# Kernel optimization log

Hardware: AMD Instinct MI355X
Metric: run time of the kernel (lower is better)

Reference implementation:

```python
import jax, jax.numpy as jnp
import numpy as np

NINP, NHID, NTOK, NLAYERS, BSZ = 4096, 512, 50257, 2, 32
T_ENC, T_DEC = 80, 40


def lstm_layer(x, h0, c0, Wih, Whh, b):
    """Single LSTM layer over a [T,B,in] sequence; PyTorch gate order i,f,g,o."""
    def step(carry, xt):
        h, c = carry
        z = xt @ Wih.T + h @ Whh.T + b  # [B, 4H]
        i, f, g, o = jnp.split(z, 4, axis=-1)
        c = jax.nn.sigmoid(f) * c + jax.nn.sigmoid(i) * jnp.tanh(g)
        h = jax.nn.sigmoid(o) * jnp.tanh(c)
        return (h, c), h
    (hN, cN), ys = jax.lax.scan(step, (h0, c0), x)
    return ys, hN, cN


def multi_lstm(x, h0, c0, params):
    """Stacked LSTM; params = list of (Wih, Whh, b) per layer."""
    hs, cs = [], []
    y = x
    for l, (Wih, Whh, b) in enumerate(params):
        y, hN, cN = lstm_layer(y, h0[l], c0[l], Wih, Whh, b)
        hs.append(hN); cs.append(cN)
    return y, jnp.stack(hs), jnp.stack(cs)


def setup_inputs():
    key = jax.random.key(0)
    ks = iter(jax.random.split(key, 32))
    def rn(shape, scale=0.05):
        return (jax.random.normal(next(ks), shape, dtype=jnp.float32) * scale)
    H4 = 4 * NHID
    d = {}
    d["inp"] = rn((T_ENC, BSZ, NINP), 1.0)
    for name in ("hid1_h", "hid1_c", "hid2_h", "hid2_c"):
        d[name] = jnp.zeros((NLAYERS, BSZ, NHID), jnp.float32)
    # lstm1: layer0 in=NINP, layer1 in=NHID (b = b_ih + b_hh fused)
    d["l1_Wih0"] = rn((H4, NINP)); d["l1_Whh0"] = rn((H4, NHID)); d["l1_b0"] = rn((H4,))
    d["l1_Wih1"] = rn((H4, NHID)); d["l1_Whh1"] = rn((H4, NHID)); d["l1_b1"] = rn((H4,))
    # lstm2: layer0 in=2*NHID, layer1 in=NHID
    d["l2_Wih0"] = rn((H4, 2 * NHID)); d["l2_Whh0"] = rn((H4, NHID)); d["l2_b0"] = rn((H4,))
    d["l2_Wih1"] = rn((H4, NHID)); d["l2_Whh1"] = rn((H4, NHID)); d["l2_b1"] = rn((H4,))
    d["W_out"] = rn((NTOK, NHID)); d["b_out"] = rn((NTOK,))
    d["W_emb"] = rn((NHID, NTOK)); d["b_emb"] = rn((NHID,))
    d["target_len"] = T_DEC
    return d


def reference(inp, hid1_h, hid1_c, hid2_h, hid2_c,
              l1_Wih0, l1_Whh0, l1_b0, l1_Wih1, l1_Whh1, l1_b1,
              l2_Wih0, l2_Whh0, l2_b0, l2_Wih1, l2_Whh1, l2_b1,
              W_out, b_out, W_emb, b_emb, target_len):
    p1 = [(l1_Wih0, l1_Whh0, l1_b0), (l1_Wih1, l1_Whh1, l1_b1)]
    p2 = [(l2_Wih0, l2_Whh0, l2_b0), (l2_Wih1, l2_Whh1, l2_b1)]
    T, B, ninp = inp.shape
    H = hid1_h.shape[-1]
    # --- encoding stage ---
    out1, h1, c1 = multi_lstm(inp, hid1_h, hid1_c, p1)
    pad_h = jnp.zeros((T, B, H), inp.dtype)
    _, h2, c2 = multi_lstm(jnp.concatenate([pad_h, out1], axis=-1), hid2_h, hid2_c, p2)
    # --- decoding stage ---
    pad_in = jnp.zeros((target_len, B, ninp), inp.dtype)
    out1d, _, _ = multi_lstm(pad_in, h1, c1, p1)
    # vocab2emb(one-hot BOS at index 0) = W_emb[:, 0] + b_emb; never updated in
    # the original loop (variable-name bug), so it is constant over decode steps,
    # making the per-step loop equivalent to one lstm2 scan.
    bos_emb = W_emb[:, 0] + b_emb  # [H]
    bos = jnp.broadcast_to(bos_emb, (target_len, B, H))
    out2d, _, _ = multi_lstm(jnp.concatenate([bos, out1d], axis=-1), h2, c2, p2)
    logits = jnp.einsum('tbh,vh->tbv', out2d, W_out) + b_out  # [T_dec, B, V]
    return jax.nn.log_softmax(logits, axis=-1)
```

## Files before the change

### kernel.cpp

```cpp
#include <hip/hip_runtime.h>
#include <hip/hip_bf16.h>
#include <cstddef>

#define NINP 4096
#define NHID 512
#define G4   2048
#define NTOK 50257
#define BSZ  32
#define T_ENC 80
#define T_DEC 40

typedef __attribute__((ext_vector_type(4))) float  f32x4;
typedef __attribute__((ext_vector_type(4))) __bf16 bf16x4;
typedef __attribute__((ext_vector_type(8))) __bf16 bf16x8;

__device__ __forceinline__ int sw_off(int r, int k) {
    return r * 128 + ((((k >> 3) ^ (r & 7)) << 4) | ((k & 7) << 1));
}
__device__ __forceinline__ int swA(int r, int k) {
    return r * 256 + ((((k >> 3) ^ (r & 7)) << 4) | ((k & 7) << 1));
}
__device__ __forceinline__ int sw512(int r, int k) {
    return r * 1024 + ((((k >> 3) ^ (r & 7)) << 4) | ((k & 7) << 1));
}

__device__ __forceinline__ bf16x4 hi4(const float4& v) {
    bf16x4 h; h[0] = (__bf16)v.x; h[1] = (__bf16)v.y;
    h[2] = (__bf16)v.z; h[3] = (__bf16)v.w; return h;
}

__device__ __forceinline__ void split8(const float4& a, const float4& b,
                                       bf16x8& h, bf16x8& l) {
    float x[8] = {a.x, a.y, a.z, a.w, b.x, b.y, b.z, b.w};
    #pragma unroll
    for (int i = 0; i < 8; i++) {
        __bf16 hb = (__bf16)x[i];
        h[i] = hb; l[i] = (__bf16)(x[i] - (float)hb);
    }
}

__device__ __forceinline__ bf16x8 to_bf16x8(const float4& a, const float4& b) {
    bf16x8 r;
    r[0]=(__bf16)a.x; r[1]=(__bf16)a.y; r[2]=(__bf16)a.z; r[3]=(__bf16)a.w;
    r[4]=(__bf16)b.x; r[5]=(__bf16)b.y; r[6]=(__bf16)b.z; r[7]=(__bf16)b.w;
    return r;
}

__device__ __forceinline__ void unpack8(const uint4& a, const uint4& b,
                                        bf16x8& h, bf16x8& l) {
    unsigned u[8] = {a.x, a.y, a.z, a.w, b.x, b.y, b.z, b.w};
    union { unsigned short s; __bf16 v; } t;
    #pragma unroll
    for (int i = 0; i < 8; i++) {
        t.s = (unsigned short)(u[i] & 0xffff); h[i] = t.v;
        t.s = (unsigned short)(u[i] >> 16);    l[i] = t.v;
    }
}
__device__ __forceinline__ bf16x8 unpack_hi8(const uint4& a, const uint4& b) {
    unsigned u[8] = {a.x, a.y, a.z, a.w, b.x, b.y, b.z, b.w};
    union { unsigned short s; __bf16 v; } t;
    bf16x8 h;
    #pragma unroll
    for (int i = 0; i < 8; i++) { t.s = (unsigned short)(u[i] & 0xffff); h[i] = t.v; }
    return h;
}

__device__ __forceinline__ unsigned pack_hilo(float x) {
    __bf16 hb = (__bf16)x;
    float hf = (float)hb;
    __bf16 lb = (__bf16)(x - hf);
    union { __bf16 b; unsigned short s; } ch, cl;
    ch.b = hb; cl.b = lb;
    return (unsigned)ch.s | ((unsigned)cl.s << 16);
}

__device__ __forceinline__ float fast_sigmoid(float x) {
    return 1.f / (1.f + __expf(-x));
}
__device__ __forceinline__ float fast_tanh(float x) {
    return 1.f - 2.f / (__expf(2.f * x) + 1.f);
}

__global__ __launch_bounds__(256) void gemm_ahi(
    const float* __restrict__ A, int lda,
    const float* __restrict__ B, int ldb,
    const float* __restrict__ bias,
    float* __restrict__ Z, int ldz,
    int N, int K)
{
    __shared__ __align__(16) char lds[32768];
    const int tid  = threadIdx.x;
    const int bm   = blockIdx.y * 128;
    const int bn   = blockIdx.x * 128;
    const int wave = tid >> 6;
    const int lane = tid & 63;
    const int wm   = (wave >> 1) * 64;
    const int wn   = (wave & 1) * 64;
    const int lr   = lane & 15;
    const int kg   = lane >> 4;

    const int rr = tid >> 4;
    const int kk = (tid & 15) * 4;

    f32x4 acc[4][4] = {};

    for (int k0 = 0; k0 < K; k0 += 64) {
        float4 av[8], bv[8];
        #pragma unroll
        for (int i = 0; i < 8; i++) {
            int r = i * 16 + rr;
            av[i] = *(const float4*)&A[(size_t)(bm + r) * lda + k0 + kk];
            int rb = bn + r;
            if (rb < N)
                bv[i] = *(const float4*)&B[(size_t)rb * ldb + k0 + kk];
            else
                bv[i] = make_float4(0.f, 0.f, 0.f, 0.f);
        }
        __syncthreads();
        #pragma unroll
        for (int i = 0; i < 8; i++) {
            int r = i * 16 + rr;
            int off = sw_off(r, kk);
            *(bf16x4*)(lds + off)         = hi4(av[i]);
            *(bf16x4*)(lds + 16384 + off) = hi4(bv[i]);
        }
        __syncthreads();
        #pragma unroll
        for (int ks = 0; ks < 2; ks++) {
            bf16x8 ah[4], bh[4];
            const int kbase = ks * 32 + kg * 8;
            #pragma unroll
            for (int f = 0; f < 4; f++) {
                ah[f] = *(const bf16x8*)(lds + sw_off(wm + f * 16 + lr, kbase));
                bh[f] = *(const bf16x8*)(lds + 16384 + sw_off(wn + f * 16 + lr, kbase));
            }
            #pragma unroll
            for (int fm = 0; fm < 4; fm++)
                #pragma unroll
                for (int fn = 0; fn < 4; fn++)
                    acc[fm][fn] = __builtin_amdgcn_mfma_f32_16x16x32_bf16(
                        ah[fm], bh[fn], acc[fm][fn], 0, 0, 0);
        }
        __syncthreads();
    }

    #pragma unroll
    for (int fn = 0; fn < 4; fn++) {
        int col = bn + wn + fn * 16 + lr;
        if (col < N) {
            float bb = bias ? bias[col] : 0.f;
            #pragma unroll
            for (int fm = 0; fm < 4; fm++) {
                #pragma unroll
                for (int j = 0; j < 4; j++) {
                    int row = bm + wm + fm * 16 + kg * 4 + j;
                    Z[(size_t)row * ldz + col] = acc[fm][fn][j] + bb;
                }
            }
        }
    }
}

__global__ __launch_bounds__(256, 1) void gemm_vocab(
    const __bf16* __restrict__ Ah,
    const float* __restrict__ B,
    const float* __restrict__ bias,
    float* __restrict__ Z)
{
    __shared__ __align__(16) char lds[163840];
    char* ldsB = lds;
    char* ldsA = lds + 131072;

    const int tid  = threadIdx.x;
    const int bn   = blockIdx.x * 128;
    const int wave = tid >> 6;
    const int lane = tid & 63;
    const int wm   = (wave >> 1) * 64;
    const int wn   = (wave & 1) * 64;
    const int lr   = lane & 15;
    const int kg   = lane >> 4;

    #pragma unroll 4
    for (int jj = 0; jj < 32; jj++) {
        int e = tid + jj * 256;
        int row = e >> 6;
        int k = (e & 63) * 8;
        int gr = bn + row;
        float4 v0, v1;
        if (gr < NTOK) {
            v0 = *(const float4*)&B[(size_t)gr * 512 + k];
            v1 = *(const float4*)&B[(size_t)gr * 512 + k + 4];
        } else {
            v0 = make_float4(0.f,0.f,0.f,0.f); v1 = v0;
        }
        *(bf16x8*)(ldsB + sw512(row, k)) = to_bf16x8(v0, v1);
    }

    float bb[4];
    #pragma unroll
    for (int fn = 0; fn < 4; fn++) {
        int col = bn + wn + fn * 16 + lr;
        bb[fn] = (col < NTOK) ? bias[col] : 0.f;
    }
    __syncthreads();

    for (int mt = 0; mt < 10; mt++) {
        f32x4 acc[4][4] = {};
        for (int k0 = 0; k0 < 4; k0++) {
            __syncthreads();
            #pragma unroll
            for (int jj = 0; jj < 8; jj++) {
                int e = tid + jj * 256;
                int row = e >> 4;
                int k = (e & 15) * 8;
                uint4 v = *(const uint4*)&Ah[(size_t)(mt * 128 + row) * 512 + k0 * 128 + k];
                *(uint4*)(ldsA + swA(row, k)) = v;
            }
            __syncthreads();
            #pragma unroll
            for (int ks = 0; ks < 4; ks++) {
                bf16x8 ah[4], bh[4];
                const int ka = ks * 32 + kg * 8;
                #pragma unroll
                for (int f = 0; f < 4; f++) {
                    ah[f] = *(const bf16x8*)(ldsA + swA(wm + f * 16 + lr, ka));
                    bh[f] = *(const bf16x8*)(ldsB + sw512(wn + f * 16 + lr, k0 * 128 + ka));
                }
                #pragma unroll
                for (int fm = 0; fm < 4; fm++)
                    #pragma unroll
                    for (int fn = 0; fn < 4; fn++)
                        acc[fm][fn] = __builtin_amdgcn_mfma_f32_16x16x32_bf16(
                            ah[fm], bh[fn], acc[fm][fn], 0, 0, 0);
            }
        }
        #pragma unroll
        for (int fn = 0; fn < 4; fn++) {
            int col = bn + wn + fn * 16 + lr;
            if (col < NTOK) {
                #pragma unroll
                for (int fm = 0; fm < 4; fm++) {
                    #pragma unroll
                    for (int j = 0; j < 4; j++) {
                        int row = mt * 128 + wm + fm * 16 + kg * 4 + j;
                        Z[(size_t)row * NTOK + col] = acc[fm][fn][j] + bb[fn];
                    }
                }
            }
        }
    }
}

__device__ __forceinline__ void grid_barrier(unsigned* flags, unsigned* gen,
                                             unsigned target)
{
    __syncthreads();
    if (threadIdx.x == 0) {
        __builtin_amdgcn_fence(__ATOMIC_RELEASE, "agent");
        __hip_atomic_store(&flags[blockIdx.x], target, __ATOMIC_RELAXED,
                           __HIP_MEMORY_SCOPE_AGENT);
    }
    if (blockIdx.x == 0) {
        while (__hip_atomic_load(&flags[threadIdx.x], __ATOMIC_RELAXED,
                                 __HIP_MEMORY_SCOPE_AGENT) < target)
            ;
        __syncthreads();
        if (threadIdx.x == 0)
            __hip_atomic_store(gen, target, __ATOMIC_RELAXED,
                               __HIP_MEMORY_SCOPE_AGENT);
    }
    if (threadIdx.x == 0) {
        while (__hip_atomic_load(gen, __ATOMIC_RELAXED,
                                 __HIP_MEMORY_SCOPE_AGENT) < target)
            __builtin_amdgcn_s_sleep(1);
        __builtin_amdgcn_fence(__ATOMIC_ACQUIRE, "agent");
    }
    __syncthreads();
}

__global__ __launch_bounds__(256, 1) void fused_scan(
    const float* __restrict__ Zx,
    const float* __restrict__ Whh_0, const float* __restrict__ bias_0,
    const float* __restrict__ Wih_1, const float* __restrict__ Whh_1,
    const float* __restrict__ bias_1,
    const float* __restrict__ Wih_2, const float* __restrict__ Whh_2,
    const float* __restrict__ bias_2e, const float* __restrict__ bias_2d,
    const float* __restrict__ Wih_3, const float* __restrict__ Whh_3,
    const float* __restrict__ bias_3,
    const float* __restrict__ hid1_h, const float* __restrict__ hid1_c,
    const float* __restrict__ hid2_h, const float* __restrict__ hid2_c,
    __bf16* __restrict__ dec3h,
    unsigned* hbuf, unsigned* flags, unsigned* gen)
{
    __shared__ __align__(16) char lds[131072];
    float* a_x = (float*)(lds + 32768);

    const int tid  = threadIdx.x;
    const int L    = blockIdx.x >> 6;
    const int bidc = blockIdx.x & 63;
    const int wave = tid >> 6;
    const int lane = tid & 63;
    const int mh   = wave >> 1;
    const int nh   = wave & 1;
    const int lr   = lane & 15;
    const int kg   = lane >> 4;
    const int jcbase = bidc * 8;
    const int bq = tid >> 3;
    const int aq = tid & 7;

    const float* Whh = (L==0)?Whh_0:(L==1)?Whh_1:(L==2)?Whh_2:Whh_3;
    const float* Wih = (L==1)?Wih_1:(L==2)?Wih_2:(L==3)?Wih_3:nullptr;
    const int ld_ih  = (L==2)?1024:512;
    const float* be  = (L==0)?bias_0:(L==1)?bias_1:(L==2)?bias_2e:bias_3;
    const float* bd  = (L==2)?bias_2d:be;
    const float* h0  = ((L<2)?hid1_h:hid2_h) + (L&1)*16384;
    const float* c0  = ((L<2)?hid1_c:hid2_c) + (L&1)*16384;
    unsigned* myb       = hbuf + L*32768;
    const unsigned* xsb = hbuf + (L>0 ? (L-1)*32768 : 0);

    {
        int gate = (bq<8)?0:(bq<16)?2:(bq<24)?1:3;
        int row  = gate*512 + jcbase + (bq&7);
        const float* wr = Whh + (size_t)row * 512;
        #pragma unroll
        for (int jj = 0; jj < 8; jj++) {
            int k = aq*8 + jj*64;
            *(bf16x8*)(lds + 65536 + sw512(bq, k)) =
                to_bf16x8(*(const float4*)(wr+k), *(const float4*)(wr+k+4));
        }
        if (Wih) {
            const float* wr2 = Wih + (size_t)row * ld_ih;
            #pragma unroll
            for (int jj = 0; jj < 8; jj++) {
                int k = aq*8 + jj*64;
                *(bf16x8*)(lds + 98304 + sw512(bq, k)) =
                    to_bf16x8(*(const float4*)(wr2+k), *(const float4*)(wr2+k+4));
            }
        }
    }

    const int n_col = nh*16 + lr;
    const int gate  = (n_col<8)?0:(n_col<16)?2:(n_col<24)?1:3;
    const int col2048 = gate*512 + jcbase + (n_col & 7);
    const float bbe = be[col2048];
    const float bbd = bd[col2048];

    float cc[4] = {0.f, 0.f, 0.f, 0.f};
    if (nh == 1 && lr < 8) {
        #pragma unroll
        for (int j = 0; j < 4; j++)
            cc[j] = c0[(mh*16 + kg*4 + j)*512 + jcbase + lr];
    }

    float zxr[4] = {0.f, 0.f, 0.f, 0.f};
    if (L == 0) {
        #pragma unroll
        for (int j = 0; j < 4; j++)
            zxr[j] = Zx[(size_t)(mh*16 + kg*4 + j)*G4 + col2048];
    }
    __syncthreads();

    const int rowA = mh*16 + lr;
    const int rowB = nh*16 + lr;

    for (int tt = 0; tt < 123; ++tt) {
        const int myt = tt - L;
        if (myt >= 0 && myt < 120) {
            uint4 xr[8][2];
            if (L > 0) {
                const unsigned* xs = xsb + (size_t)(myt & 1)*16384 + bq*512;
                #pragma unroll
                for (int jj = 0; jj < 8; jj++) {
                    int k = aq*8 + jj*64;
                    xr[jj][0] = *(const uint4*)(xs + k);
                    xr[jj][1] = *(const uint4*)(xs + k + 4);
                }
            }
            if (myt == 0) {
                const float* hr = h0 + bq*512;
                #pragma unroll
                for (int jj = 0; jj < 8; jj++) {
                    int k = aq*8 + jj*64;
                    bf16x8 H, Lo;
                    split8(*(const float4*)(hr+k), *(const float4*)(hr+k+4), H, Lo);
                    int off = sw512(bq, k);
                    *(bf16x8*)(lds + off)         = H;
                    *(bf16x8*)(lds + 32768 + off) = Lo;
                }
            } else {
                const unsigned* hs = myb + (size_t)((myt-1) & 1)*16384 + bq*512;
                #pragma unroll
                for (int jj = 0; jj < 8; jj++) {
                    int k = aq*8 + jj*64;
                    bf16x8 H, Lo;
                    unpack8(*(const uint4*)(hs+k), *(const uint4*)(hs+k+4), H, Lo);
                    int off = sw512(bq, k);
                    *(bf16x8*)(lds + off)         = H;
                    *(bf16x8*)(lds + 32768 + off) = Lo;
                }
            }
            __syncthreads();

            f32x4 accA = {0.f,0.f,0.f,0.f}, accB = {0.f,0.f,0.f,0.f};
            #pragma unroll
            for (int ks = 0; ks < 16; ++ks) {
                int k = ks*32 + kg*8;
                int offA = sw512(rowA, k);
                int offB = sw512(rowB, k);
                bf16x8 ah = *(const bf16x8*)(lds + offA);
                bf16x8 al = *(const bf16x8*)(lds + 32768 + offA);
                bf16x8 bh = *(const bf16x8*)(lds + 65536 + offB);
                accA = __builtin_amdgcn_mfma_f32_16x16x32_bf16(ah, bh, accA, 0,0,0);
                accB = __builtin_amdgcn_mfma_f32_16x16x32_bf16(al, bh, accB, 0,0,0);
            }
            __syncthreads();

            if (L > 0) {
                #pragma unroll
                for (int jj = 0; jj < 8; jj++) {
                    int k = aq*8 + jj*64;
                    *(bf16x8*)(lds + sw512(bq, k)) = unpack_hi8(xr[jj][0], xr[jj][1]);
                }
                __syncthreads();
                #pragma unroll
                for (int ks = 0; ks < 16; ++ks) {
                    int k = ks*32 + kg*8;
                    bf16x8 ax = *(const bf16x8*)(lds + sw512(rowA, k));
                    bf16x8 bi = *(const bf16x8*)(lds + 98304 + sw512(rowB, k));
                    accA = __builtin_amdgcn_mfma_f32_16x16x32_bf16(ax, bi, accA, 0,0,0);
                }
            }

            const float bbv = (L == 2 && myt >= 80) ? bbd : bbe;
            float z[4];
            #pragma unroll
            for (int j = 0; j < 4; j++)
                z[j] = accA[j] + accB[j] + bbv
                     + ((L == 0 && myt < 80) ? zxr[j] : 0.f);

            {
                int mytn = myt + 1;
                if (L == 0 && mytn < 80) {
                    #pragma unroll
                    for (int j = 0; j < 4; j++)
                        zxr[j] = Zx[(size_t)mytn*(BSZ*G4)
                                    + (mh*16+kg*4+j)*G4 + col2048];
                }
            }

            if (nh == 0) {
                float zo[4];
                #pragma unroll
                for (int j = 0; j < 4; j++) zo[j] = __shfl_xor(z[j], 8);
                if (lr < 8) {
                    #pragma unroll
                    for (int j = 0; j < 4; j++)
                        a_x[(mh*16 + kg*4 + j)*8 + lr] =
                            fast_sigmoid(z[j]) * fast_tanh(zo[j]);
                }
            }
            __syncthreads();

            if (nh == 1) {
                float cnew[4] = {0.f,0.f,0.f,0.f};
                if (lr < 8) {
                    #pragma unroll
                    for (int j = 0; j < 4; j++) {
                        float av = a_x[(mh*16 + kg*4 + j)*8 + lr];
                        cnew[j] = fast_sigmoid(z[j]) * cc[j] + av;
                        cc[j] = cnew[j];
                    }
                }
                float cfrom[4];
                #pragma unroll
                for (int j = 0; j < 4; j++) cfrom[j] = __shfl_xor(cnew[j], 8);
                if (lr >= 8) {
                    #pragma unroll
                    for (int j = 0; j < 4; j++) {
                        float hn = fast_sigmoid(z[j]) * fast_tanh(cfrom[j]);
                        int b = mh*16 + kg*4 + j;
                        int hcol = jcbase + (lr - 8);
                        if (L == 3 && myt >= 80)
                            dec3h[(size_t)(myt-80)*(BSZ*NHID) + b*512 + hcol] =
                                (__bf16)hn;
                        __hip_atomic_store(&myb[(size_t)(myt & 1)*16384 + b*512 + hcol],
                                           pack_hilo(hn), __ATOMIC_RELAXED,
                                           __HIP_MEMORY_SCOPE_AGENT);
                    }
                }
            }
        }
        grid_barrier(flags, gen, (unsigned)tt + 1u);
    }
}

__global__ __launch_bounds__(256) void bias2_kernel(
    const float* __restrict__ W_emb,
    const float* __restrict__ b_emb,
    const float* __restrict__ Wih0,
    const float* __restrict__ b0,
    float* __restrict__ bias2)
{
    __shared__ float bos[NHID];
    const int tid = threadIdx.x;
    for (int i = tid; i < NHID; i += 256)
        bos[i] = W_emb[(size_t)i * NTOK] + b_emb[i];
    __syncthreads();
    int j = blockIdx.x * 256 + tid;
    float acc = b0[j];
    for (int k = 0; k < NHID; k++)
        acc += bos[k] * Wih0[(size_t)j * 1024 + k];
    bias2[j] = acc;
}

__global__ __launch_bounds__(256) void logsoftmax_kernel(float* __restrict__ logits)
{
    const size_t row = blockIdx.x;
    float* p = logits + row * (size_t)NTOK;
    const int tid = threadIdx.x;

    float m = -1e30f, s = 0.f;
    for (int i = tid; i < NTOK; i += 256) {
        float x = p[i];
        float mn = fmaxf(m, x);
        s = s * __expf(m - mn) + __expf(x - mn);
        m = mn;
    }
    #pragma unroll
    for (int off = 32; off > 0; off >>= 1) {
        float mo = __shfl_down(m, off);
        float so = __shfl_down(s, off);
        float mn = fmaxf(m, mo);
        s = s * __expf(m - mn) + so * __expf(mo - mn);
        m = mn;
    }
    __shared__ float sm[4], ss[4];
    if ((tid & 63) == 0) { sm[tid >> 6] = m; ss[tid >> 6] = s; }
    __syncthreads();
    float M4 = fmaxf(fmaxf(sm[0], sm[1]), fmaxf(sm[2], sm[3]));
    float S  = ss[0] * __expf(sm[0] - M4) + ss[1] * __expf(sm[1] - M4)
             + ss[2] * __expf(sm[2] - M4) + ss[3] * __expf(sm[3] - M4);
    float lse = M4 + logf(S);
    for (int i = tid; i < NTOK; i += 256) p[i] = p[i] - lse;
}

extern "C" void kernel_launch(void* const* d_in, const int* in_sizes, int n_in,
                              void* d_out, int out_size, void* d_ws, size_t ws_size,
                              hipStream_t stream)
{
    const float* inp     = (const float*)d_in[0];
    const float* hid1_h  = (const float*)d_in[1];
    const float* hid1_c  = (const float*)d_in[2];
    const float* hid2_h  = (const float*)d_in[3];
    const float* hid2_c  = (const float*)d_in[4];
    const float* l1_Wih0 = (const float*)d_in[5];
    const float* l1_Whh0 = (const float*)d_in[6];
    const float* l1_b0   = (const float*)d_in[7];
    const float* l1_Wih1 = (const float*)d_in[8];
    const float* l1_Whh1 = (const float*)d_in[9];
    const float* l1_b1   = (const float*)d_in[10];
    const float* l2_Wih0 = (const float*)d_in[11];
    const float* l2_Whh0 = (const float*)d_in[12];
    const float* l2_b0   = (const float*)d_in[13];
    const float* l2_Wih1 = (const float*)d_in[14];
    const float* l2_Whh1 = (const float*)d_in[15];
    const float* l2_b1   = (const float*)d_in[16];
    const float* W_out   = (const float*)d_in[17];
    const float* b_out   = (const float*)d_in[18];
    const float* W_emb   = (const float*)d_in[19];
    const float* b_emb   = (const float*)d_in[20];

    float* out = (float*)d_out;
    float* ws  = (float*)d_ws;

    float* Zx    = ws;
    float* bias2 = ws + 5242880;
    __bf16* dec3h = (__bf16*)(ws + 5244928);
    unsigned* hbuf  = (unsigned*)(ws + 5572608);
    unsigned* flags = (unsigned*)(ws + 5703680);
    unsigned* gen   = flags + 256;

    (void)hipMemsetAsync(flags, 0, 1028, stream);

    {
        dim3 grid((G4 + 127) / 128, (T_ENC * BSZ) / 128);
        gemm_ahi<<<grid, dim3(256), 0, stream>>>(
            inp, NINP, l1_Wih0, NINP, nullptr, Zx, G4, G4, NINP);
    }
    bias2_kernel<<<8, 256, 0, stream>>>(W_emb, b_emb, l2_Wih0, l2_b0, bias2);

    fused_scan<<<256, 256, 0, stream>>>(
        Zx,
        l1_Whh0, l1_b0,
        l1_Wih1, l1_Whh1, l1_b1,
        l2_Wih0 + 512, l2_Whh0, l2_b0, bias2,
        l2_Wih1, l2_Whh1, l2_b1,
        hid1_h, hid1_c, hid2_h, hid2_c,
        dec3h, hbuf, flags, gen);

    gemm_vocab<<<(NTOK + 127) / 128, dim3(256), 0, stream>>>(
        dec3h, W_out, b_out, out);
    logsoftmax_kernel<<<1280, dim3(256), 0, stream>>>(out);
}
```

Baseline: 1.914 ms.

## Shrink vocab GEMM tile to 64 columns for two blocks per CU; vectorize log-softmax

The vocab projection kernel now uses 64-column N tiles with half the LDS (80KB), so two blocks fit per CU, doubling the grid to about 786 blocks and staging A in 64-wide K chunks. This is meant to improve occupancy and load balance across CUs at the cost of reloading the A panel twice as often per output column. The log-softmax kernel switches to aligned float4 loads and stores with scalar head and tail handling. Its online max/sum update now takes a branch so the common case costs a single exp.

```diff
diff --git a/kernel.cpp b/kernel.cpp
--- a/kernel.cpp
+++ b/kernel.cpp
@@ -16,9 +16,6 @@
 
 __device__ __forceinline__ int sw_off(int r, int k) {
     return r * 128 + ((((k >> 3) ^ (r & 7)) << 4) | ((k & 7) << 1));
-}
-__device__ __forceinline__ int swA(int r, int k) {
-    return r * 256 + ((((k >> 3) ^ (r & 7)) << 4) | ((k & 7) << 1));
 }
 __device__ __forceinline__ int sw512(int r, int k) {
     return r * 1024 + ((((k >> 3) ^ (r & 7)) << 4) | ((k & 7) << 1));
@@ -161,27 +158,27 @@
     }
 }
 
-__global__ __launch_bounds__(256, 1) void gemm_vocab(
+__global__ __launch_bounds__(256, 2) void gemm_vocab64(
     const __bf16* __restrict__ Ah,
     const float* __restrict__ B,
     const float* __restrict__ bias,
     float* __restrict__ Z)
 {
-    __shared__ __align__(16) char lds[163840];
+    __shared__ __align__(16) char lds[81920];
     char* ldsB = lds;
-    char* ldsA = lds + 131072;
+    char* ldsA = lds + 65536;
 
     const int tid  = threadIdx.x;
-    const int bn   = blockIdx.x * 128;
+    const int bn   = blockIdx.x * 64;
     const int wave = tid >> 6;
     const int lane = tid & 63;
     const int wm   = (wave >> 1) * 64;
-    const int wn   = (wave & 1) * 64;
+    const int wn   = (wave & 1) * 32;
     const int lr   = lane & 15;
     const int kg   = lane >> 4;
 
     #pragma unroll 4
-    for (int jj = 0; jj < 32; jj++) {
+    for (int jj = 0; jj < 16; jj++) {
         int e = tid + jj * 256;
         int row = e >> 6;
         int k = (e & 63) * 8;
@@ -196,46 +193,47 @@
         *(bf16x8*)(ldsB + sw512(row, k)) = to_bf16x8(v0, v1);
     }
 
-    float bb[4];
+    float bb[2];
     #pragma unroll
-    for (int fn = 0; fn < 4; fn++) {
+    for (int fn = 0; fn < 2; fn++) {
         int col = bn + wn + fn * 16 + lr;
         bb[fn] = (col < NTOK) ? bias[col] : 0.f;
     }
     __syncthreads();
 
     for (int mt = 0; mt < 10; mt++) {
-        f32x4 acc[4][4] = {};
-        for (int k0 = 0; k0 < 4; k0++) {
+        f32x4 acc[4][2] = {};
+        for (int k0 = 0; k0 < 8; k0++) {
             __syncthreads();
             #pragma unroll
-            for (int jj = 0; jj < 8; jj++) {
+            for (int jj = 0; jj < 4; jj++) {
                 int e = tid + jj * 256;
-                int row = e >> 4;
-                int k = (e & 15) * 8;
-                uint4 v = *(const uint4*)&Ah[(size_t)(mt * 128 + row) * 512 + k0 * 128 + k];
-                *(uint4*)(ldsA + swA(row, k)) = v;
+                int row = e >> 3;
+                int k = (e & 7) * 8;
+                uint4 v = *(const uint4*)&Ah[(size_t)(mt * 128 + row) * 512 + k0 * 64 + k];
+                *(uint4*)(ldsA + sw_off(row, k)) = v;
             }
             __syncthreads();
             #pragma unroll
-            for (int ks = 0; ks < 4; ks++) {
-                bf16x8 ah[4], bh[4];
+            for (int ks = 0; ks < 2; ks++) {
+                bf16x8 ah[4], bh[2];
                 const int ka = ks * 32 + kg * 8;
                 #pragma unroll
-                for (int f = 0; f < 4; f++) {
-                    ah[f] = *(const bf16x8*)(ldsA + swA(wm + f * 16 + lr, ka));
-                    bh[f] = *(const bf16x8*)(ldsB + sw512(wn + f * 16 + lr, k0 * 128 + ka));
-                }
+                for (int f = 0; f < 4; f++)
+                    ah[f] = *(const bf16x8*)(ldsA + sw_off(wm + f * 16 + lr, ka));
+                #pragma unroll
+                for (int f = 0; f < 2; f++)
+                    bh[f] = *(const bf16x8*)(ldsB + sw512(wn + f * 16 + lr, k0 * 64 + ka));
                 #pragma unroll
                 for (int fm = 0; fm < 4; fm++)
                     #pragma unroll
-                    for (int fn = 0; fn < 4; fn++)
+                    for (int fn = 0; fn < 2; fn++)
                         acc[fm][fn] = __builtin_amdgcn_mfma_f32_16x16x32_bf16(
                             ah[fm], bh[fn], acc[fm][fn], 0, 0, 0);
             }
         }
         #pragma unroll
-        for (int fn = 0; fn < 4; fn++) {
+        for (int fn = 0; fn < 2; fn++) {
             int col = bn + wn + fn * 16 + lr;
             if (col < NTOK) {
                 #pragma unroll
@@ -519,13 +517,28 @@
     float* p = logits + row * (size_t)NTOK;
     const int tid = threadIdx.x;
 
+    const int head = (int)((4 - (((size_t)row * NTOK) & 3)) & 3);
+    const int nv   = (NTOK - head) >> 2;
+    const int tail = head + nv * 4;
+    float4* p4 = (float4*)(p + head);
+
     float m = -1e30f, s = 0.f;
-    for (int i = tid; i < NTOK; i += 256) {
-        float x = p[i];
-        float mn = fmaxf(m, x);
-        s = s * __expf(m - mn) + __expf(x - mn);
-        m = mn;
-    }
+    auto upd = [&](float x) {
+        if (x <= m) {
+            s += __expf(x - m);
+        } else {
+            s = s * __expf(m - x) + 1.f;
+            m = x;
+        }
+    };
+
+    for (int i = tid; i < head; i += 256) upd(p[i]);
+    for (int i = tid; i < nv; i += 256) {
+        float4 v = p4[i];
+        upd(v.x); upd(v.y); upd(v.z); upd(v.w);
+    }
+    for (int i = tail + tid; i < NTOK; i += 256) upd(p[i]);
+
     #pragma unroll
     for (int off = 32; off > 0; off >>= 1) {
         float mo = __shfl_down(m, off);
@@ -541,7 +554,14 @@
     float S  = ss[0] * __expf(sm[0] - M4) + ss[1] * __expf(sm[1] - M4)
              + ss[2] * __expf(sm[2] - M4) + ss[3] * __expf(sm[3] - M4);
     float lse = M4 + logf(S);
-    for (int i = tid; i < NTOK; i += 256) p[i] = p[i] - lse;
+
+    for (int i = tid; i < head; i += 256) p[i] -= lse;
+    for (int i = tid; i < nv; i += 256) {
+        float4 v = p4[i];
+        v.x -= lse; v.y -= lse; v.z -= lse; v.w -= lse;
+        p4[i] = v;
+    }
+    for (int i = tail + tid; i < NTOK; i += 256) p[i] -= lse;
 }
 
 extern "C" void kernel_launch(void* const* d_in, const int* in_sizes, int n_in,
@@ -598,7 +618,7 @@
         hid1_h, hid1_c, hid2_h, hid2_c,
         dec3h, hbuf, flags, gen);
 
-    gemm_vocab<<<(NTOK + 127) / 128, dim3(256), 0, stream>>>(
+    gemm_vocab64<<<(NTOK + 63) / 64, dim3(256), 0, stream>>>(
         dec3h, W_out, b_out, out);
     logsoftmax_kernel<<<1280, dim3(256), 0, stream>>>(out);
 }
```

Result: faster. 1.815 ms, median of 2 (-5.2%).
